# Optimization experiments

Measured on AMD Instinct MI355X. Metric: run time of the kernel, lower is better.

Reference implementation:

```python
import jax, jax.numpy as jnp
import numpy as np

L, B, E = 2048, 4, 1024
H = 8
D1 = 2048          # expand_ratio * E, multiple of H
HD = D1 // H       # head dim 256
MAX_L = 2048
EPS = 1e-8


def setup_inputs() -> dict:
    key = jax.random.key(0)
    ks = jax.random.split(key, 9)
    std = 0.02
    return {
        "x": jax.random.normal(ks[0], (L, B, E), jnp.float32),
        "Wu": jax.random.normal(ks[1], (D1, E), jnp.float32) * std,
        "bu": jax.random.normal(ks[2], (D1,), jnp.float32) * std,
        "Wv": jax.random.normal(ks[3], (D1, E), jnp.float32) * std,
        "bv": jax.random.normal(ks[4], (D1,), jnp.float32) * std,
        "Wo": jax.random.normal(ks[5], (E, D1), jnp.float32) * std,
        "bo": jax.random.normal(ks[6], (E,), jnp.float32) * std,
        "zero": jax.random.normal(ks[7], (H, 1), jnp.float32) * 0.1,   # Toeplitz coef, offset 0
        "pos": jax.random.normal(ks[8], (H, MAX_L - 1), jnp.float32) * 0.1,  # offsets 1..n-1
    }


def _simple_rmsnorm(x):
    d = x.shape[-1]
    rms = jnp.linalg.norm(x, axis=-1, keepdims=True) * (d ** -0.5)
    return x / (rms + EPS)


def _toeplitz_causal_fft(v, zero, pos):
    # v: (b, h, n, hd); causal Toeplitz mixing along n via FFT long conv
    n = v.shape[-2]
    coef = jnp.concatenate([zero, pos[:, : n - 1]], axis=-1)  # (h, n)
    m = 2 * n
    cf = jnp.fft.rfft(coef, m, axis=-1)                  # (h, m//2+1)
    vf = jnp.fft.rfft(v, m, axis=-2)                     # (b, h, m//2+1, hd)
    out = jnp.fft.irfft(cf[None, :, :, None] * vf, m, axis=-2)
    return out[:, :, :n, :]


def reference(x, Wu, bu, Wv, bv, Wo, bo, zero, pos):
    # x: (n, b, e) fairseq layout
    n, b, e = x.shape
    shortcut = x
    xn = _simple_rmsnorm(x)                               # pre_norm (SimpleRMSNorm, no params)
    u = jax.nn.silu(jnp.einsum('nbe,de->nbd', xn, Wu) + bu)   # (n,b,d1)
    v = jax.nn.silu(jnp.einsum('nbe,de->nbd', xn, Wv) + bv)   # (n,b,d1)
    # 'n b (h d) -> b h n d'
    vh = v.transpose(1, 0, 2).reshape(b, n, H, HD).transpose(0, 2, 1, 3)
    oh = _toeplitz_causal_fft(vh, zero, pos)              # (b,h,n,hd)
    o = oh.transpose(0, 2, 1, 3).reshape(b, n, D1).transpose(1, 0, 2)  # (n,b,d1)
    o = u * o                                             # gating
    out = jnp.einsum('nbd,ed->nbe', o, Wo) + bo + shortcut
    return out
```

## Files before the change

### kernel.cpp

```cpp
#include <hip/hip_runtime.h>
#include <cstdint>
#include <cstddef>

#define LQ   2048
#define BQ   4
#define EQ   1024
#define HQ   8
#define D1Q  2048
#define HDQ  256
#define NBQ  (LQ*BQ)

typedef __bf16 bf16_t;
typedef __bf16 bf16x8 __attribute__((ext_vector_type(8)));
typedef __bf16 bf16x4 __attribute__((ext_vector_type(4)));
typedef float  f32x4  __attribute__((ext_vector_type(4)));

#define GAS1(p) ((const __attribute__((address_space(1))) void*)(p))
#define LAS3(p) ((__attribute__((address_space(3))) void*)(p))


__global__ __launch_bounds__(256) void convert_kernel(
    const float* __restrict__ Wu, const float* __restrict__ Wv,
    const float* __restrict__ Wo,
    bf16_t* __restrict__ Wub, bf16_t* __restrict__ Wvb,
    bf16_t* __restrict__ Wob)
{
    const size_t i = (size_t)blockIdx.x * 256 + threadIdx.x;
    if (i < (size_t)D1Q * EQ) {
        Wub[i] = (bf16_t)Wu[i];
        Wvb[i] = (bf16_t)Wv[i];
        Wob[i] = (bf16_t)Wo[i];
    }
}

__global__ __launch_bounds__(256) void build_toep_tiles2(
    const float* __restrict__ zero, const float* __restrict__ pos,
    bf16_t* __restrict__ At)
{
    const int q = blockIdx.x;
    const int h = blockIdx.y;
    const int doff = (q - 1) * 64;
    const int tid = threadIdx.x;
    bf16_t* dst = At + ((size_t)h * 32 + q) * 8192;
    const int r  = tid >> 1;
    const int c0 = (tid & 1) * 32;
    bf16_t vals[32];
    #pragma unroll
    for (int j = 0; j < 32; ++j) {
        const int d = doff + r - (c0 + j);
        float v = 0.f;
        if (d == 0) v = zero[h];
        else if (d > 0 && d < LQ) v = pos[(size_t)h * (LQ - 1) + d - 1];
        vals[j] = (bf16_t)v;
    }
    #pragma unroll
    for (int qq = 0; qq < 4; ++qq)
        *(bf16x8*)(dst + r * 64 + c0 + qq * 8) = *(bf16x8*)(vals + qq * 8);
}

__global__ __launch_bounds__(256) void rmsnorm_kernel(
    const float* __restrict__ x, bf16_t* __restrict__ xn)
{
    const int row = blockIdx.x;
    const int tid = threadIdx.x;
    const float4 v = ((const float4*)(x + (size_t)row * EQ))[tid];
    float ss = v.x*v.x + v.y*v.y + v.z*v.z + v.w*v.w;
    #pragma unroll
    for (int m = 32; m >= 1; m >>= 1) ss += __shfl_xor(ss, m, 64);
    __shared__ float red[4];
    const int wid = tid >> 6, lane = tid & 63;
    if (lane == 0) red[wid] = ss;
    __syncthreads();
    const float tot = red[0] + red[1] + red[2] + red[3];
    const float inv = 1.f / (sqrtf(tot * (1.f / EQ)) + 1e-8f);
    bf16x4 o;
    o[0] = (bf16_t)(v.x * inv); o[1] = (bf16_t)(v.y * inv);
    o[2] = (bf16_t)(v.z * inv); o[3] = (bf16_t)(v.w * inv);
    *(bf16x4*)(xn + (size_t)row * EQ + tid * 4) = o;
}


template<int KK, int MH, int WAITN, bool LDB, int MI_, typename F>
__device__ __forceinline__ void phase_op(const char* base, int offA0, int offB0,
    bf16x8 (&bv)[4], f32x4 (&acc)[MI_][4], F&& stage)
{
    bf16x8 av[4];
    #pragma unroll
    for (int i = 0; i < 4; ++i)
        av[i] = *(const bf16x8*)(base + (offA0 ^ (KK << 6)) + (MH * 4 + i) * 2048);
    if constexpr (LDB) {
        #pragma unroll
        for (int i = 0; i < 4; ++i)
            bv[i] = *(const bf16x8*)(base + (offB0 ^ (KK << 6)) + i * 2048);
    }
    stage();
    __builtin_amdgcn_s_barrier();
    __builtin_amdgcn_s_setprio(1);
    #pragma unroll
    for (int i = 0; i < 4; ++i)
        #pragma unroll
        for (int ni = 0; ni < 4; ++ni)
            acc[MH * 4 + i][ni] = __builtin_amdgcn_mfma_f32_16x16x32_bf16(
                av[i], bv[ni], acc[MH * 4 + i][ni], 0, 0, 0);
    __builtin_amdgcn_s_setprio(0);
    if constexpr (WAITN >= 0)
        asm volatile("s_waitcnt vmcnt(%0)" :: "i"(WAITN) : "memory");
    __builtin_amdgcn_s_barrier();
}


template<int MODE>
__global__ __launch_bounds__(512, 1) void gemm_big(
    const bf16_t* __restrict__ A, const bf16_t* __restrict__ Bm,
    int K, int N, const float* __restrict__ bias, bf16_t* __restrict__ Cb)
{
    constexpr int BSTRIDE = 65536;
    __shared__ alignas(16) char smem[2 * BSTRIDE];

    const int nwg   = gridDim.x * gridDim.y;
    const int bid0  = blockIdx.y * gridDim.x + blockIdx.x;
    const int chunkw = nwg >> 3;
    const int sb    = (bid0 & 7) * chunkw + (bid0 >> 3);
    const int bx    = sb % gridDim.x;
    const int by    = sb / gridDim.x;

    const int tid  = threadIdx.x;
    const int wid  = tid >> 6;
    const int lane = tid & 63;
    const int frow = lane & 15;
    const int c    = lane >> 4;
    const int m0 = by * 256;
    const int n0 = bx * 256;
    const int wrm = (wid >> 2) * 128;
    const int wrn = (wid & 3) * 64;

    const int g = frow & 7;
    const int offA0 = (wrm + frow) * 128 + ((c ^ g) << 4);
    const int offB0 = 32768 + (wrn + frow) * 128 + ((c ^ g) << 4);

    const int rl = tid >> 3;
    const int ls = (tid & 7) ^ (rl & 7);
    const size_t lda2 = (size_t)K * 2;
    const char* sA = (const char*)A  + (size_t)(m0 + rl) * lda2 + ls * 16;
    const char* sB = (const char*)Bm + (size_t)(n0 + rl) * lda2 + ls * 16;

    auto SH = [&](int bf, int op, int hf, int kt) {
        const char* s = (op ? sB : sA) + (size_t)(hf * 128) * lda2 + (size_t)kt * 128;
        char* d = smem + bf * BSTRIDE + op * 32768 + hf * 16384 + wid * 1024;
        __builtin_amdgcn_global_load_lds(GAS1(s), LAS3(d), 16, 0, 0);
        __builtin_amdgcn_global_load_lds(GAS1(s + 64 * lda2), LAS3(d + 8192), 16, 0, 0);
    };

    f32x4 acc[8][4];
    #pragma unroll
    for (int i = 0; i < 8; ++i)
        #pragma unroll
        for (int j = 0; j < 4; ++j) acc[i][j] = (f32x4){0.f, 0.f, 0.f, 0.f};
    bf16x8 bv[4];

    const int NT = K >> 6;

    SH(0,0,0,0); SH(0,0,1,0); SH(0,1,0,0); SH(0,1,1,0); SH(1,1,0,1);
    asm volatile("s_waitcnt vmcnt(2)" ::: "memory");
    __builtin_amdgcn_s_barrier();

    const char* b0 = smem;
    const char* b1 = smem + BSTRIDE;
    for (int i = 0; i < NT / 2; ++i) {
        const int t1 = 2 * i + 1, t2 = 2 * i + 2;
        const bool p2 = t2 < NT, p3 = t2 + 1 < NT;
        phase_op<0,0,-1,true >(b0, offA0, offB0, bv, acc, [&]{ SH(1,1,1,t1); });
        phase_op<0,1,-1,false>(b0, offA0, offB0, bv, acc, [&]{ SH(1,0,0,t1); });
        phase_op<1,0,-1,true >(b0, offA0, offB0, bv, acc, [&]{ SH(1,0,1,t1); });
        phase_op<1,1, 2,false>(b0, offA0, offB0, bv, acc, [&]{ if (p2) SH(0,1,0,t2); });
        phase_op<0,0,-1,true >(b1, offA0, offB0, bv, acc, [&]{ if (p2) SH(0,1,1,t2); });
        phase_op<0,1,-1,false>(b1, offA0, offB0, bv, acc, [&]{ if (p2) SH(0,0,0,t2); });
        phase_op<1,0,-1,true >(b1, offA0, offB0, bv, acc, [&]{ if (p2) SH(0,0,1,t2); });
        phase_op<1,1, 2,false>(b1, offA0, offB0, bv, acc, [&]{ if (p3) SH(1,1,0,t2+1); });
    }

    if constexpr (MODE == 1) {
        const int hh = n0 >> 8;
        float bb[4];
        #pragma unroll
        for (int ni = 0; ni < 4; ++ni) bb[ni] = bias[n0 + wrn + ni * 16 + frow];

        #pragma unroll
        for (int p = 0; p < 2; ++p) {
            __syncthreads();
            bf16_t* chunk = (bf16_t*)smem + wid * 4224;
            #pragma unroll
            for (int mi = 0; mi < 8; ++mi) {
                #pragma unroll
                for (int nio = 0; nio < 2; ++nio) {
                    const int ni = p * 2 + nio;
                    const int nl = nio * 16 + frow;
                    #pragma unroll
                    for (int j = 0; j < 4; ++j) {
                        float v = acc[mi][ni][j] + bb[ni];
                        v = v / (1.f + __expf(-v));
                        chunk[nl * 132 + j * 32 + mi * 4 + c] = (bf16_t)v;
                    }
                }
            }
            __syncthreads();
            const int nl  = lane & 31;
            const int bh2 = lane >> 5;
            const int hd  = wrn + p * 32 + nl;
            const int t0  = (m0 + wrm) >> 2;
            #pragma unroll
            for (int bi = 0; bi < 2; ++bi) {
                const int b2 = bh2 * 2 + bi;
                const bf16_t* src = chunk + nl * 132 + b2 * 32;
                bf16_t* dst = Cb + (((size_t)hh * 4 + b2) * 256 + hd) * (size_t)LQ + t0;
                #pragma unroll
                for (int q = 0; q < 4; ++q)
                    *(bf16x8*)(dst + q * 8) = *(const bf16x8*)(src + q * 8);
            }
        }
        return;
    }

    const int fq = c * 4;
    #pragma unroll
    for (int mi = 0; mi < 8; ++mi) {
        #pragma unroll
        for (int ni = 0; ni < 4; ++ni) {
            const int gn = n0 + wrn + ni * 16 + frow;
            #pragma unroll
            for (int j = 0; j < 4; ++j) {
                const int gm = m0 + wrm + mi * 16 + fq + j;
                float v = acc[mi][ni][j] + bias[gn];
                v = v / (1.f + __expf(-v));
                Cb[(size_t)gm * N + gn] = (bf16_t)v;
            }
        }
    }
}

__global__ __launch_bounds__(512, 1) void gemm_fin(
    const bf16_t* __restrict__ A, const bf16_t* __restrict__ Bm,
    const float* __restrict__ bias, const float* __restrict__ res,
    float* __restrict__ Cf)
{
    constexpr int K = D1Q, N = EQ;
    constexpr int BSTRIDE = 49152;
    __shared__ alignas(16) char smem[3 * BSTRIDE];

    const int nwg   = gridDim.x * gridDim.y;
    const int bid0  = blockIdx.y * gridDim.x + blockIdx.x;
    const int chunkw = nwg >> 3;
    const int sb    = (bid0 & 7) * chunkw + (bid0 >> 3);
    const int bx    = sb % gridDim.x;
    const int by    = sb / gridDim.x;

    const int tid  = threadIdx.x;
    const int wid  = tid >> 6;
    const int lane = tid & 63;
    const int frow = lane & 15;
    const int c    = lane >> 4;
    const int m0 = by * 128;
    const int n0 = bx * 256;
    const int wrm = (wid >> 2) * 64;
    const int wrn = (wid & 3) * 64;

    const int g = frow & 7;
    const int offA0 = (wrm + frow) * 128 + ((c ^ g) << 4);
    const int offB0 = 16384 + (wrn + frow) * 128 + ((c ^ g) << 4);

    const int rl = tid >> 3;
    const int ls = (tid & 7) ^ (rl & 7);
    const size_t lda2 = (size_t)K * 2;
    const char* sA = (const char*)A  + (size_t)(m0 + rl) * lda2 + ls * 16;
    const char* sB = (const char*)Bm + (size_t)(n0 + rl) * lda2 + ls * 16;

    auto SH_A = [&](int bf, int kt) {
        const char* s = sA + (size_t)kt * 128;
        char* d = smem + bf * BSTRIDE + wid * 1024;
        __builtin_amdgcn_global_load_lds(GAS1(s), LAS3(d), 16, 0, 0);
        __builtin_amdgcn_global_load_lds(GAS1(s + 64 * lda2), LAS3(d + 8192), 16, 0, 0);
    };
    auto SH_B = [&](int bf, int hf, int kt) {
        const char* s = sB + (size_t)(hf * 128) * lda2 + (size_t)kt * 128;
        char* d = smem + bf * BSTRIDE + 16384 + hf * 16384 + wid * 1024;
        __builtin_amdgcn_global_load_lds(GAS1(s), LAS3(d), 16, 0, 0);
        __builtin_amdgcn_global_load_lds(GAS1(s + 64 * lda2), LAS3(d + 8192), 16, 0, 0);
    };

    f32x4 acc[4][4];
    #pragma unroll
    for (int i = 0; i < 4; ++i)
        #pragma unroll
        for (int j = 0; j < 4; ++j) acc[i][j] = (f32x4){0.f, 0.f, 0.f, 0.f};
    bf16x8 bv[4];

    const int NT = K >> 6;

    SH_A(0, 0); SH_B(0, 0, 0); SH_B(0, 1, 0);
    SH_A(1, 1); SH_B(1, 0, 1); SH_B(1, 1, 1);
    asm volatile("s_waitcnt vmcnt(6)" ::: "memory");
    __builtin_amdgcn_s_barrier();

    int cur = 0, pb = 2;
    for (int t = 0; t < NT; ++t) {
        const char* base = smem + cur * BSTRIDE;
        const int t2 = t + 2;
        const bool pf = t2 < NT;
        phase_op<0,0,-1,true>(base, offA0, offB0, bv, acc,
            [&]{ if (pf) { SH_A(pb, t2); SH_B(pb, 0, t2); } });
        phase_op<1,0, 6,true>(base, offA0, offB0, bv, acc,
            [&]{ if (pf) SH_B(pb, 1, t2); });
        cur = (cur == 2) ? 0 : cur + 1;
        pb  = (pb  == 2) ? 0 : pb  + 1;
    }

    const int fq = c * 4;
    #pragma unroll
    for (int mi = 0; mi < 4; ++mi) {
        #pragma unroll
        for (int ni = 0; ni < 4; ++ni) {
            const int gn = n0 + wrn + ni * 16 + frow;
            #pragma unroll
            for (int j = 0; j < 4; ++j) {
                const int gm = m0 + wrm + mi * 16 + fq + j;
                Cf[(size_t)gm * N + gn] =
                    acc[mi][ni][j] + bias[gn] + res[(size_t)gm * N + gn];
            }
        }
    }
}

__global__ __launch_bounds__(512, 1) void gemm_toep4p(
    const bf16_t* __restrict__ VT, const bf16_t* __restrict__ Atl,
    const bf16_t* __restrict__ U, bf16_t* __restrict__ O)
{
    constexpr int BSTRIDE = 49152;
    __shared__ alignas(16) char smem[3 * BSTRIDE];

    const int bid   = blockIdx.x;
    const int m_blk = 15 - (bid >> 5);
    const int sub   = bid & 31;
    const int h     = sub >> 2;
    const int n0    = (sub & 3) * 256;
    const int m0    = m_blk * 128;

    const int tid  = threadIdx.x;
    const int wid  = tid >> 6;
    const int lane = tid & 63;
    const int frow = lane & 15;
    const int c    = lane >> 4;
    const int wrm  = (wid >> 2) * 64;
    const int wrn  = (wid & 3) * 64;

    const int g = frow & 7;
    const int offA0 = (wrm + frow) * 128 + ((c ^ g) << 4);
    const int offB0 = 16384 + (wrn + frow) * 128 + ((c ^ g) << 4);

    const int rl = tid >> 3;
    const int ls = (tid & 7) ^ (rl & 7);
    const char* Ah = (const char*)Atl + (size_t)h * 32 * 16384;
    const size_t ldb = (size_t)LQ * 2;
    const char* sB = (const char*)VT + ((size_t)h * 1024 + n0 + rl) * ldb + ls * 16;

    auto SH_A = [&](int bf, int kt) {
        const int q = 2 * m_blk - kt + 1;
        const char* s = Ah + (size_t)q * 16384 + (size_t)rl * 128 + ls * 16;
        char* d = smem + bf * BSTRIDE + wid * 1024;
        __builtin_amdgcn_global_load_lds(GAS1(s), LAS3(d), 16, 0, 0);
        __builtin_amdgcn_global_load_lds(GAS1(s + 64 * 128), LAS3(d + 8192), 16, 0, 0);
    };
    auto SH_B = [&](int bf, int hf, int kt) {
        const char* s = sB + (size_t)(hf * 128) * ldb + (size_t)kt * 128;
        char* d = smem + bf * BSTRIDE + 16384 + hf * 16384 + wid * 1024;
        __builtin_amdgcn_global_load_lds(GAS1(s), LAS3(d), 16, 0, 0);
        __builtin_amdgcn_global_load_lds(GAS1(s + 64 * ldb), LAS3(d + 8192), 16, 0, 0);
    };

    f32x4 acc[4][4];
    #pragma unroll
    for (int i = 0; i < 4; ++i)
        #pragma unroll
        for (int j = 0; j < 4; ++j) acc[i][j] = (f32x4){0.f, 0.f, 0.f, 0.f};
    bf16x8 bv[4];

    const int NT = 2 * m_blk + 2;

    SH_A(0, 0); SH_B(0, 0, 0); SH_B(0, 1, 0);
    SH_A(1, 1); SH_B(1, 0, 1); SH_B(1, 1, 1);
    asm volatile("s_waitcnt vmcnt(6)" ::: "memory");
    __builtin_amdgcn_s_barrier();

    int cur = 0, pb = 2;
    for (int t = 0; t < NT; ++t) {
        const char* base = smem + cur * BSTRIDE;
        const int t2 = t + 2;
        const bool pf = t2 < NT;
        phase_op<0,0,-1,true>(base, offA0, offB0, bv, acc,
            [&]{ if (pf) { SH_A(pb, t2); SH_B(pb, 0, t2); } });
        phase_op<1,0, 6,true>(base, offA0, offB0, bv, acc,
            [&]{ if (pf) SH_B(pb, 1, t2); });
        cur = (cur == 2) ? 0 : cur + 1;
        pb  = (pb  == 2) ? 0 : pb  + 1;
    }

    const int fq = c * 4;
    #pragma unroll
    for (int mi = 0; mi < 4; ++mi) {
        #pragma unroll
        for (int ni = 0; ni < 4; ++ni) {
            const int nn = n0 + wrn + ni * 16 + frow;
            const int b  = nn >> 8, hd = nn & 255;
            #pragma unroll
            for (int j = 0; j < 4; ++j) {
                const int t = m0 + wrm + mi * 16 + fq + j;
                const size_t idx = ((size_t)t * BQ + b) * D1Q + h * HDQ + hd;
                const float uval = (float)U[idx];
                O[idx] = (bf16_t)(uval * acc[mi][ni][j]);
            }
        }
    }
}


extern "C" void kernel_launch(void* const* d_in, const int* in_sizes, int n_in,
                              void* d_out, int out_size, void* d_ws, size_t ws_size,
                              hipStream_t stream)
{
    const float* x    = (const float*)d_in[0];
    const float* Wu   = (const float*)d_in[1];
    const float* bu   = (const float*)d_in[2];
    const float* Wv   = (const float*)d_in[3];
    const float* bv   = (const float*)d_in[4];
    const float* Wo   = (const float*)d_in[5];
    const float* bo   = (const float*)d_in[6];
    const float* zero = (const float*)d_in[7];
    const float* pos  = (const float*)d_in[8];
    float* out = (float*)d_out;

    char* ws = (char*)d_ws;
    size_t off = 0;
    auto alloc = [&](size_t bytes) {
        char* p = ws + off;
        off += (bytes + 255) & ~(size_t)255;
        return p;
    };
    bf16_t* xn     = (bf16_t*)alloc((size_t)NBQ * EQ * 2);
    bf16_t* Wub    = (bf16_t*)alloc((size_t)D1Q * EQ * 2);
    bf16_t* Wvb    = (bf16_t*)alloc((size_t)D1Q * EQ * 2);
    bf16_t* Wob    = (bf16_t*)alloc((size_t)EQ * D1Q * 2);
    bf16_t* Atiles = (bf16_t*)alloc((size_t)HQ * 32 * 8192 * 2);
    bf16_t* Ub     = (bf16_t*)alloc((size_t)NBQ * D1Q * 2);
    bf16_t* VTb    = (bf16_t*)alloc((size_t)NBQ * D1Q * 2);
    bf16_t* Ob     = (bf16_t*)alloc((size_t)NBQ * D1Q * 2);

    convert_kernel<<<8192, 256, 0, stream>>>(Wu, Wv, Wo, Wub, Wvb, Wob);
    build_toep_tiles2<<<dim3(32, 8), 256, 0, stream>>>(zero, pos, Atiles);
    rmsnorm_kernel<<<NBQ, 256, 0, stream>>>(x, xn);

    dim3 g1(D1Q / 256, NBQ / 256);
    gemm_big<0><<<g1, 512, 0, stream>>>(xn, Wub, EQ, D1Q, bu, Ub);
    gemm_big<1><<<g1, 512, 0, stream>>>(xn, Wvb, EQ, D1Q, bv, VTb);

    gemm_toep4p<<<512, 512, 0, stream>>>(VTb, Atiles, Ub, Ob);

    dim3 g2(EQ / 256, NBQ / 128);
    gemm_fin<<<g2, 512, 0, stream>>>(Ob, Wob, bo, x, out);
}
```

Measured before the change: 198.2 us.

## Fuse U and V projection GEMMs into a single 1024-thread pipelined kernel

Result: slower. 202.4 us (+2.1%).

```diff
diff --git a/kernel.cpp b/kernel.cpp
--- a/kernel.cpp
+++ b/kernel.cpp
@@ -79,6 +79,148 @@
     *(bf16x4*)(xn + (size_t)row * EQ + tid * 4) = o;
 }
 
+__global__ __launch_bounds__(1024, 1) void gemm_uv(
+    const bf16_t* __restrict__ A, const bf16_t* __restrict__ Bm,
+    const float* __restrict__ bbu, const float* __restrict__ bbv,
+    bf16_t* __restrict__ Ub, bf16_t* __restrict__ Vt)
+{
+    constexpr int K = EQ;
+    constexpr int BSTRIDE = 32768;
+    __shared__ alignas(16) char smem[4 * BSTRIDE];
+
+    const int nwg  = gridDim.x * gridDim.y;
+    const int bid0 = blockIdx.y * gridDim.x + blockIdx.x;
+    const int chunkw = nwg >> 3;
+    const int sb   = (bid0 & 7) * chunkw + (bid0 >> 3);
+    const int bx   = sb % gridDim.x;
+    const int by   = sb / gridDim.x;
+
+    const int tid  = threadIdx.x;
+    const int wid  = tid >> 6;
+    const int lane = tid & 63;
+    const int frow = lane & 15;
+    const int c    = lane >> 4;
+    const int m0 = by * 256;
+    const int n0 = bx * 256;
+    const int wrm = (wid >> 2) * 64;
+    const int wrn = (wid & 3) * 64;
+
+    const int g = (frow >> 1) & 3;
+    const int offA0 = (wrm + frow) * 64 + ((c ^ g) << 4);
+    const int offB0 = 16384 + (wrn + frow) * 64 + ((c ^ g) << 4);
+
+    const int rA   = tid >> 2;
+    const int soff = (((tid & 3) ^ ((rA >> 1) & 3)) << 4);
+    const size_t lda2 = (size_t)K * 2;
+    const char* sA = (const char*)A  + (size_t)(m0 + rA) * lda2 + soff;
+    const char* sB = (const char*)Bm + (size_t)(n0 + rA) * lda2 + soff;
+
+    auto STAGE = [&](int bf, int kt) {
+        char* d = smem + bf * BSTRIDE + wid * 1024;
+        __builtin_amdgcn_global_load_lds(GAS1(sA + (size_t)kt * 64), LAS3(d), 16, 0, 0);
+        __builtin_amdgcn_global_load_lds(GAS1(sB + (size_t)kt * 64), LAS3(d + 16384), 16, 0, 0);
+    };
+
+    f32x4 acc[4][4];
+    #pragma unroll
+    for (int i = 0; i < 4; ++i)
+        #pragma unroll
+        for (int j = 0; j < 4; ++j) acc[i][j] = (f32x4){0.f, 0.f, 0.f, 0.f};
+
+    const int NT = K >> 5;
+
+    STAGE(0, 0); STAGE(1, 1); STAGE(2, 2);
+    asm volatile("s_waitcnt vmcnt(4)" ::: "memory");
+    __builtin_amdgcn_s_barrier();
+
+    for (int t = 0; t < NT; ++t) {
+        const char* base = smem + (t & 3) * BSTRIDE;
+        bf16x8 av[4], bfr[4];
+        #pragma unroll
+        for (int i = 0; i < 4; ++i) {
+            av[i]  = *(const bf16x8*)(base + offA0 + i * 1024);
+            bfr[i] = *(const bf16x8*)(base + offB0 + i * 1024);
+        }
+        if (t + 3 < NT) STAGE((t + 3) & 3, t + 3);
+        __builtin_amdgcn_s_setprio(1);
+        #pragma unroll
+        for (int mi = 0; mi < 4; ++mi)
+            #pragma unroll
+            for (int ni = 0; ni < 4; ++ni)
+                acc[mi][ni] = __builtin_amdgcn_mfma_f32_16x16x32_bf16(
+                    av[mi], bfr[ni], acc[mi][ni], 0, 0, 0);
+        __builtin_amdgcn_s_setprio(0);
+        if (t + 3 < NT)      asm volatile("s_waitcnt vmcnt(4)" ::: "memory");
+        else if (t + 2 < NT) asm volatile("s_waitcnt vmcnt(2)" ::: "memory");
+        else if (t + 1 < NT) asm volatile("s_waitcnt vmcnt(0)" ::: "memory");
+        if (t + 1 < NT) __builtin_amdgcn_s_barrier();
+    }
+
+    if (bx < 8) {
+        const int fq = c * 4;
+        #pragma unroll
+        for (int mi = 0; mi < 4; ++mi) {
+            #pragma unroll
+            for (int ni = 0; ni < 4; ++ni) {
+                const int gn = n0 + wrn + ni * 16 + frow;
+                #pragma unroll
+                for (int j = 0; j < 4; ++j) {
+                    const int gm = m0 + wrm + mi * 16 + fq + j;
+                    float v = acc[mi][ni][j] + bbu[gn];
+                    v = v / (1.f + __expf(-v));
+                    Ub[(size_t)gm * D1Q + gn] = (bf16_t)v;
+                }
+            }
+        }
+        return;
+    }
+
+    {
+        const int n0v = n0 - 2048;
+        const int hh  = n0v >> 8;
+        float bb[4];
+        #pragma unroll
+        for (int ni = 0; ni < 4; ++ni) bb[ni] = bbv[n0v + wrn + ni * 16 + frow];
+
+        const int pi   = wid & 3;
+        const int q    = (wid >> 2) & 1;
+        const int pass = wid >> 3;
+        bf16_t* chunk = (bf16_t*)smem + pi * 8448;
+
+        #pragma unroll
+        for (int p = 0; p < 2; ++p) {
+            __syncthreads();
+            if (pass == p) {
+                #pragma unroll
+                for (int mi = 0; mi < 4; ++mi)
+                    #pragma unroll
+                    for (int ni = 0; ni < 4; ++ni) {
+                        const int nl = ni * 16 + frow;
+                        #pragma unroll
+                        for (int j = 0; j < 4; ++j) {
+                            float v = acc[mi][ni][j] + bb[ni];
+                            v = v / (1.f + __expf(-v));
+                            chunk[nl * 132 + j * 32 + q * 16 + mi * 4 + c] = (bf16_t)v;
+                        }
+                    }
+            }
+            __syncthreads();
+            if (pass == p) {
+                const int hd = wrn + lane;
+                const int t0 = (m0 >> 2) + p * 32;
+                #pragma unroll
+                for (int bi = 0; bi < 2; ++bi) {
+                    const int b2 = q * 2 + bi;
+                    const bf16_t* src = chunk + lane * 132 + b2 * 32;
+                    bf16_t* dst = Vt + (((size_t)hh * 4 + b2) * 256 + hd) * (size_t)LQ + t0;
+                    #pragma unroll
+                    for (int u = 0; u < 4; ++u)
+                        *(bf16x8*)(dst + u * 8) = *(const bf16x8*)(src + u * 8);
+                }
+            }
+        }
+    }
+}
 
 template<int KK, int MH, int WAITN, bool LDB, int MI_, typename F>
 __device__ __forceinline__ void phase_op(const char* base, int offA0, int offB0,
@@ -106,136 +248,6 @@
     if constexpr (WAITN >= 0)
         asm volatile("s_waitcnt vmcnt(%0)" :: "i"(WAITN) : "memory");
     __builtin_amdgcn_s_barrier();
-}
-
-
-template<int MODE>
-__global__ __launch_bounds__(512, 1) void gemm_big(
-    const bf16_t* __restrict__ A, const bf16_t* __restrict__ Bm,
-    int K, int N, const float* __restrict__ bias, bf16_t* __restrict__ Cb)
-{
-    constexpr int BSTRIDE = 65536;
-    __shared__ alignas(16) char smem[2 * BSTRIDE];
-
-    const int nwg   = gridDim.x * gridDim.y;
-    const int bid0  = blockIdx.y * gridDim.x + blockIdx.x;
-    const int chunkw = nwg >> 3;
-    const int sb    = (bid0 & 7) * chunkw + (bid0 >> 3);
-    const int bx    = sb % gridDim.x;
-    const int by    = sb / gridDim.x;
-
-    const int tid  = threadIdx.x;
-    const int wid  = tid >> 6;
-    const int lane = tid & 63;
-    const int frow = lane & 15;
-    const int c    = lane >> 4;
-    const int m0 = by * 256;
-    const int n0 = bx * 256;
-    const int wrm = (wid >> 2) * 128;
-    const int wrn = (wid & 3) * 64;
-
-    const int g = frow & 7;
-    const int offA0 = (wrm + frow) * 128 + ((c ^ g) << 4);
-    const int offB0 = 32768 + (wrn + frow) * 128 + ((c ^ g) << 4);
-
-    const int rl = tid >> 3;
-    const int ls = (tid & 7) ^ (rl & 7);
-    const size_t lda2 = (size_t)K * 2;
-    const char* sA = (const char*)A  + (size_t)(m0 + rl) * lda2 + ls * 16;
-    const char* sB = (const char*)Bm + (size_t)(n0 + rl) * lda2 + ls * 16;
-
-    auto SH = [&](int bf, int op, int hf, int kt) {
-        const char* s = (op ? sB : sA) + (size_t)(hf * 128) * lda2 + (size_t)kt * 128;
-        char* d = smem + bf * BSTRIDE + op * 32768 + hf * 16384 + wid * 1024;
-        __builtin_amdgcn_global_load_lds(GAS1(s), LAS3(d), 16, 0, 0);
-        __builtin_amdgcn_global_load_lds(GAS1(s + 64 * lda2), LAS3(d + 8192), 16, 0, 0);
-    };
-
-    f32x4 acc[8][4];
-    #pragma unroll
-    for (int i = 0; i < 8; ++i)
-        #pragma unroll
-        for (int j = 0; j < 4; ++j) acc[i][j] = (f32x4){0.f, 0.f, 0.f, 0.f};
-    bf16x8 bv[4];
-
-    const int NT = K >> 6;
-
-    SH(0,0,0,0); SH(0,0,1,0); SH(0,1,0,0); SH(0,1,1,0); SH(1,1,0,1);
-    asm volatile("s_waitcnt vmcnt(2)" ::: "memory");
-    __builtin_amdgcn_s_barrier();
-
-    const char* b0 = smem;
-    const char* b1 = smem + BSTRIDE;
-    for (int i = 0; i < NT / 2; ++i) {
-        const int t1 = 2 * i + 1, t2 = 2 * i + 2;
-        const bool p2 = t2 < NT, p3 = t2 + 1 < NT;
-        phase_op<0,0,-1,true >(b0, offA0, offB0, bv, acc, [&]{ SH(1,1,1,t1); });
-        phase_op<0,1,-1,false>(b0, offA0, offB0, bv, acc, [&]{ SH(1,0,0,t1); });
-        phase_op<1,0,-1,true >(b0, offA0, offB0, bv, acc, [&]{ SH(1,0,1,t1); });
-        phase_op<1,1, 2,false>(b0, offA0, offB0, bv, acc, [&]{ if (p2) SH(0,1,0,t2); });
-        phase_op<0,0,-1,true >(b1, offA0, offB0, bv, acc, [&]{ if (p2) SH(0,1,1,t2); });
-        phase_op<0,1,-1,false>(b1, offA0, offB0, bv, acc, [&]{ if (p2) SH(0,0,0,t2); });
-        phase_op<1,0,-1,true >(b1, offA0, offB0, bv, acc, [&]{ if (p2) SH(0,0,1,t2); });
-        phase_op<1,1, 2,false>(b1, offA0, offB0, bv, acc, [&]{ if (p3) SH(1,1,0,t2+1); });
-    }
-
-    if constexpr (MODE == 1) {
-        const int hh = n0 >> 8;
-        float bb[4];
-        #pragma unroll
-        for (int ni = 0; ni < 4; ++ni) bb[ni] = bias[n0 + wrn + ni * 16 + frow];
-
-        #pragma unroll
-        for (int p = 0; p < 2; ++p) {
-            __syncthreads();
-            bf16_t* chunk = (bf16_t*)smem + wid * 4224;
-            #pragma unroll
-            for (int mi = 0; mi < 8; ++mi) {
-                #pragma unroll
-                for (int nio = 0; nio < 2; ++nio) {
-                    const int ni = p * 2 + nio;
-                    const int nl = nio * 16 + frow;
-                    #pragma unroll
-                    for (int j = 0; j < 4; ++j) {
-                        float v = acc[mi][ni][j] + bb[ni];
-                        v = v / (1.f + __expf(-v));
-                        chunk[nl * 132 + j * 32 + mi * 4 + c] = (bf16_t)v;
-                    }
-                }
-            }
-            __syncthreads();
-            const int nl  = lane & 31;
-            const int bh2 = lane >> 5;
-            const int hd  = wrn + p * 32 + nl;
-            const int t0  = (m0 + wrm) >> 2;
-            #pragma unroll
-            for (int bi = 0; bi < 2; ++bi) {
-                const int b2 = bh2 * 2 + bi;
-                const bf16_t* src = chunk + nl * 132 + b2 * 32;
-                bf16_t* dst = Cb + (((size_t)hh * 4 + b2) * 256 + hd) * (size_t)LQ + t0;
-                #pragma unroll
-                for (int q = 0; q < 4; ++q)
-                    *(bf16x8*)(dst + q * 8) = *(const bf16x8*)(src + q * 8);
-            }
-        }
-        return;
-    }
-
-    const int fq = c * 4;
-    #pragma unroll
-    for (int mi = 0; mi < 8; ++mi) {
-        #pragma unroll
-        for (int ni = 0; ni < 4; ++ni) {
-            const int gn = n0 + wrn + ni * 16 + frow;
-            #pragma unroll
-            for (int j = 0; j < 4; ++j) {
-                const int gm = m0 + wrm + mi * 16 + fq + j;
-                float v = acc[mi][ni][j] + bias[gn];
-                v = v / (1.f + __expf(-v));
-                Cb[(size_t)gm * N + gn] = (bf16_t)v;
-            }
-        }
-    }
 }
 
 __global__ __launch_bounds__(512, 1) void gemm_fin(
@@ -457,9 +469,8 @@
     build_toep_tiles2<<<dim3(32, 8), 256, 0, stream>>>(zero, pos, Atiles);
     rmsnorm_kernel<<<NBQ, 256, 0, stream>>>(x, xn);
 
-    dim3 g1(D1Q / 256, NBQ / 256);
-    gemm_big<0><<<g1, 512, 0, stream>>>(xn, Wub, EQ, D1Q, bu, Ub);
-    gemm_big<1><<<g1, 512, 0, stream>>>(xn, Wvb, EQ, D1Q, bv, VTb);
+    dim3 g1(16, NBQ / 256);
+    gemm_uv<<<g1, 1024, 0, stream>>>(xn, Wub, bu, bv, Ub, VTb);
 
     gemm_toep4p<<<512, 512, 0, stream>>>(VTb, Atiles, Ub, Ob);
 
```

## Fuse U and V projection GEMMs into one launch and restage prefetch schedule

Applied to the files above, without the earlier changes.

New measurement: 198.0 us. No clear change (-0.1%).

```diff
diff --git a/kernel.cpp b/kernel.cpp
--- a/kernel.cpp
+++ b/kernel.cpp
@@ -79,7 +79,6 @@
     *(bf16x4*)(xn + (size_t)row * EQ + tid * 4) = o;
 }
 
-
 template<int KK, int MH, int WAITN, bool LDB, int MI_, typename F>
 __device__ __forceinline__ void phase_op(const char* base, int offA0, int offB0,
     bf16x8 (&bv)[4], f32x4 (&acc)[MI_][4], F&& stage)
@@ -108,12 +107,12 @@
     __builtin_amdgcn_s_barrier();
 }
 
-
-template<int MODE>
-__global__ __launch_bounds__(512, 1) void gemm_big(
+__global__ __launch_bounds__(512, 1) void gemm_uv8p(
     const bf16_t* __restrict__ A, const bf16_t* __restrict__ Bm,
-    int K, int N, const float* __restrict__ bias, bf16_t* __restrict__ Cb)
-{
+    const float* __restrict__ bbu, const float* __restrict__ bbv,
+    bf16_t* __restrict__ Ub, bf16_t* __restrict__ Vt)
+{
+    constexpr int K = EQ;
     constexpr int BSTRIDE = 65536;
     __shared__ alignas(16) char smem[2 * BSTRIDE];
 
@@ -160,30 +159,57 @@
 
     const int NT = K >> 6;
 
-    SH(0,0,0,0); SH(0,0,1,0); SH(0,1,0,0); SH(0,1,1,0); SH(1,1,0,1);
-    asm volatile("s_waitcnt vmcnt(2)" ::: "memory");
+    SH(0,0,0,0); SH(0,0,1,0); SH(0,1,0,0); SH(0,1,1,0);
+    SH(1,1,0,1); SH(1,1,1,1);
+    asm volatile("s_waitcnt vmcnt(4)" ::: "memory");
     __builtin_amdgcn_s_barrier();
 
     const char* b0 = smem;
     const char* b1 = smem + BSTRIDE;
     for (int i = 0; i < NT / 2; ++i) {
-        const int t1 = 2 * i + 1, t2 = 2 * i + 2;
-        const bool p2 = t2 < NT, p3 = t2 + 1 < NT;
-        phase_op<0,0,-1,true >(b0, offA0, offB0, bv, acc, [&]{ SH(1,1,1,t1); });
-        phase_op<0,1,-1,false>(b0, offA0, offB0, bv, acc, [&]{ SH(1,0,0,t1); });
-        phase_op<1,0,-1,true >(b0, offA0, offB0, bv, acc, [&]{ SH(1,0,1,t1); });
-        phase_op<1,1, 2,false>(b0, offA0, offB0, bv, acc, [&]{ if (p2) SH(0,1,0,t2); });
-        phase_op<0,0,-1,true >(b1, offA0, offB0, bv, acc, [&]{ if (p2) SH(0,1,1,t2); });
-        phase_op<0,1,-1,false>(b1, offA0, offB0, bv, acc, [&]{ if (p2) SH(0,0,0,t2); });
-        phase_op<1,0,-1,true >(b1, offA0, offB0, bv, acc, [&]{ if (p2) SH(0,0,1,t2); });
-        phase_op<1,1, 2,false>(b1, offA0, offB0, bv, acc, [&]{ if (p3) SH(1,1,0,t2+1); });
-    }
-
-    if constexpr (MODE == 1) {
-        const int hh = n0 >> 8;
+        const int t1 = 2 * i + 1, t2 = 2 * i + 2, t3 = 2 * i + 3;
+        const bool s2 = t2 < NT;
+        phase_op<0,0,-1,true >(b0, offA0, offB0, bv, acc,
+            [&]{ SH(1,0,0,t1); SH(1,0,1,t1); });
+        phase_op<0,1,-1,false>(b0, offA0, offB0, bv, acc, [&]{});
+        phase_op<1,0,-1,true >(b0, offA0, offB0, bv, acc, [&]{});
+        if (s2) phase_op<1,1, 4,false>(b0, offA0, offB0, bv, acc,
+            [&]{ SH(0,1,0,t2); SH(0,1,1,t2); });
+        else    phase_op<1,1, 0,false>(b0, offA0, offB0, bv, acc, [&]{});
+        phase_op<0,0,-1,true >(b1, offA0, offB0, bv, acc,
+            [&]{ if (s2) { SH(0,0,0,t2); SH(0,0,1,t2); } });
+        phase_op<0,1,-1,false>(b1, offA0, offB0, bv, acc, [&]{});
+        phase_op<1,0,-1,true >(b1, offA0, offB0, bv, acc, [&]{});
+        if (s2) phase_op<1,1, 4,false>(b1, offA0, offB0, bv, acc,
+            [&]{ SH(1,1,0,t3); SH(1,1,1,t3); });
+        else    phase_op<1,1,-1,false>(b1, offA0, offB0, bv, acc, [&]{});
+    }
+
+    if (bx < 8) {
+        const int fq = c * 4;
+        #pragma unroll
+        for (int mi = 0; mi < 8; ++mi) {
+            #pragma unroll
+            for (int ni = 0; ni < 4; ++ni) {
+                const int gn = n0 + wrn + ni * 16 + frow;
+                #pragma unroll
+                for (int j = 0; j < 4; ++j) {
+                    const int gm = m0 + wrm + mi * 16 + fq + j;
+                    float v = acc[mi][ni][j] + bbu[gn];
+                    v = v / (1.f + __expf(-v));
+                    Ub[(size_t)gm * D1Q + gn] = (bf16_t)v;
+                }
+            }
+        }
+        return;
+    }
+
+    {
+        const int n0v = n0 - 2048;
+        const int hh  = n0v >> 8;
         float bb[4];
         #pragma unroll
-        for (int ni = 0; ni < 4; ++ni) bb[ni] = bias[n0 + wrn + ni * 16 + frow];
+        for (int ni = 0; ni < 4; ++ni) bb[ni] = bbv[n0v + wrn + ni * 16 + frow];
 
         #pragma unroll
         for (int p = 0; p < 2; ++p) {
@@ -212,27 +238,10 @@
             for (int bi = 0; bi < 2; ++bi) {
                 const int b2 = bh2 * 2 + bi;
                 const bf16_t* src = chunk + nl * 132 + b2 * 32;
-                bf16_t* dst = Cb + (((size_t)hh * 4 + b2) * 256 + hd) * (size_t)LQ + t0;
+                bf16_t* dst = Vt + (((size_t)hh * 4 + b2) * 256 + hd) * (size_t)LQ + t0;
                 #pragma unroll
                 for (int q = 0; q < 4; ++q)
                     *(bf16x8*)(dst + q * 8) = *(const bf16x8*)(src + q * 8);
-            }
-        }
-        return;
-    }
-
-    const int fq = c * 4;
-    #pragma unroll
-    for (int mi = 0; mi < 8; ++mi) {
-        #pragma unroll
-        for (int ni = 0; ni < 4; ++ni) {
-            const int gn = n0 + wrn + ni * 16 + frow;
-            #pragma unroll
-            for (int j = 0; j < 4; ++j) {
-                const int gm = m0 + wrm + mi * 16 + fq + j;
-                float v = acc[mi][ni][j] + bias[gn];
-                v = v / (1.f + __expf(-v));
-                Cb[(size_t)gm * N + gn] = (bf16_t)v;
             }
         }
     }
@@ -457,9 +466,8 @@
     build_toep_tiles2<<<dim3(32, 8), 256, 0, stream>>>(zero, pos, Atiles);
     rmsnorm_kernel<<<NBQ, 256, 0, stream>>>(x, xn);
 
-    dim3 g1(D1Q / 256, NBQ / 256);
-    gemm_big<0><<<g1, 512, 0, stream>>>(xn, Wub, EQ, D1Q, bu, Ub);
-    gemm_big<1><<<g1, 512, 0, stream>>>(xn, Wvb, EQ, D1Q, bv, VTb);
+    dim3 g1(16, NBQ / 256);
+    gemm_uv8p<<<g1, 512, 0, stream>>>(xn, Wub, bu, bv, Ub, VTb);
 
     gemm_toep4p<<<512, 512, 0, stream>>>(VTb, Atiles, Ub, Ob);
 
```
